# Kernel optimization log

Hardware: AMD Instinct MI355X
Metric: run time of the kernel (lower is better)

Reference implementation:

```python
import jax, jax.numpy as jnp
import numpy as np

NUM_Q = 4096     # num_of_questions
MAX_STEP = 256   # max_step
BATCH = 64       # students per batch


def setup_inputs() -> dict:
    key = jax.random.key(0)
    k1, k2, k3, k4, k5, k6 = jax.random.split(key, 6)
    # simulated interaction sequences with random leading padding (all-zero rows)
    q_ids = jax.random.randint(k1, (BATCH, MAX_STEP), 0, NUM_Q)
    correct = jax.random.bernoulli(k2, 0.6, (BATCH, MAX_STEP)).astype(jnp.float32)
    start = jax.random.randint(k3, (BATCH,), 0, 16)  # leading pad length per student
    valid = (jnp.arange(MAX_STEP)[None, :] >= start[:, None]).astype(jnp.float32)
    oh = jax.nn.one_hot(q_ids, NUM_Q, dtype=jnp.float32)  # [B,S,Q]
    # batch = [one-hot if answered correctly | one-hot if answered incorrectly]
    batch = jnp.concatenate(
        [oh * (correct * valid)[..., None], oh * ((1.0 - correct) * valid)[..., None]],
        axis=-1,
    )  # [B,S,2Q]
    pred = jax.random.uniform(k4, (BATCH, MAX_STEP, NUM_Q), minval=0.01, maxval=0.99)
    target_q = jax.random.uniform(k5, (BATCH, 1), minval=0.01, maxval=0.99)
    target_label = jax.random.bernoulli(k6, 0.5, (BATCH,)).astype(jnp.float32)
    return {"pred": pred, "target_q": target_q, "batch": batch, "target_label": target_label}


def _bce(p, a):
    # elementwise BCE matching torch.nn.BCELoss (log clamped at -100)
    logp = jnp.maximum(jnp.log(p), -100.0)
    log1mp = jnp.maximum(jnp.log1p(-p), -100.0)
    return -(a * logp + (1.0 - a) * log1mp)


def reference(pred, target_q, batch, target_label):
    Q, S = NUM_Q, MAX_STEP
    delta = batch[:, :, :Q] + batch[:, :, Q:]  # [B,S,Q] one-hot of asked question
    # temp.gather(0, arange) extracts the diagonal of pred[:S-1] @ delta[1:].T,
    # i.e. p[s,j] = pred[s,j] . delta[s,j+1]
    p = jnp.einsum('bsq,bsq->bs', pred[:, :S - 1], delta[:, 1:])  # [B,S-1]
    # correctness label: 1 if correct, 0 if incorrect or padded ('//' is non-diff)
    a = jax.lax.stop_gradient(
        jnp.floor(((batch[:, :, :Q] - batch[:, :, Q:]).sum(-1) + 1.0) / 2.0)
    )[:, 1:]  # [B,S-1]
    # the break loop trims everything before the first p[i] > 0;
    # if no p > 0, argmax returns 0 == no trim (matching torch, where break never fires)
    i = jnp.argmax(p > 0, axis=1)  # [B]
    mask = jnp.arange(S - 1)[None, :] >= i[:, None]
    seq_loss = jnp.sum(jnp.where(mask, _bce(p, a), 0.0), axis=1)  # [B]
    tail = _bce(target_q[:, 0], target_label)  # [B]
    # per-student mean over (trimmed length + 1 appended target)
    n = ((S - 1) - i + 1).astype(pred.dtype)
    return jnp.sum((seq_loss + tail) / n)
```

## Files before the change

### kernel.cpp

```cpp
#include <hip/hip_runtime.h>
#include <limits.h>

#define NUM_Q    4096
#define MAX_STEP 256
#define BATCH    64
#define TWOQ     8192

__global__ void __launch_bounds__(256) find_onehot_kernel(
        const float* __restrict__ batch, int* __restrict__ qa) {
    const int row = blockIdx.x;
    const float4* rp = (const float4*)(batch + (size_t)row * TWOQ);

    __shared__ int found;
    if (threadIdx.x == 0) found = -1;
    __syncthreads();

    #pragma unroll
    for (int it = 0; it < 8; ++it) {
        const int vi = it * 256 + threadIdx.x;
        const float4 v = rp[vi];
        if (v.x != 0.f || v.y != 0.f || v.z != 0.f || v.w != 0.f) {
            const int base = vi * 4;
            int idx = (v.x != 0.f) ? base
                    : (v.y != 0.f) ? base + 1
                    : (v.z != 0.f) ? base + 2
                                   : base + 3;
            found = idx;
        }
    }
    __syncthreads();
    if (threadIdx.x == 0) qa[row] = found;
}

__device__ __forceinline__ float bce(float p, float a) {
    float lp  = fmaxf(logf(p), -100.0f);
    float l1p = fmaxf(log1pf(-p), -100.0f);
    return -(a * lp + (1.0f - a) * l1p);
}

__global__ void __launch_bounds__(256) loss_kernel(
        const float* __restrict__ pred,
        const float* __restrict__ target_q,
        const float* __restrict__ target_label,
        const int* __restrict__ qa,
        float* __restrict__ out) {
    const int b = blockIdx.x;
    const int t = threadIdx.x;
    const int SM1 = MAX_STEP - 1;

    __shared__ int   smin[256];
    __shared__ float ssum[256];

    int   idx = -1;
    float p   = 0.0f;
    float a   = 0.0f;
    if (t < SM1) {
        idx = qa[b * MAX_STEP + t + 1];
        if (idx >= 0) {
            const int qid = idx & (NUM_Q - 1);
            p = pred[((size_t)b * MAX_STEP + t) * NUM_Q + qid];
            a = (idx < NUM_Q) ? 1.0f : 0.0f;
        }
    }

    smin[t] = (t < SM1 && idx >= 0 && p > 0.0f) ? t : INT_MAX;
    __syncthreads();
    #pragma unroll
    for (int off = 128; off > 0; off >>= 1) {
        if (t < off) smin[t] = min(smin[t], smin[t + off]);
        __syncthreads();
    }
    const int i0 = (smin[0] == INT_MAX) ? 0 : smin[0];

    float v = 0.0f;
    if (t < SM1 && t >= i0) v = bce(p, a);
    ssum[t] = v;
    __syncthreads();
    #pragma unroll
    for (int off = 128; off > 0; off >>= 1) {
        if (t < off) ssum[t] += ssum[t + off];
        __syncthreads();
    }

    if (t == 0) {
        const float tail = bce(target_q[b], target_label[b]);
        const float n = (float)(MAX_STEP - i0);
        atomicAdd(out, (ssum[0] + tail) / n);
    }
}

extern "C" void kernel_launch(void* const* d_in, const int* in_sizes, int n_in,
                              void* d_out, int out_size, void* d_ws, size_t ws_size,
                              hipStream_t stream) {
    const float* pred         = (const float*)d_in[0];
    const float* target_q     = (const float*)d_in[1];
    const float* batch        = (const float*)d_in[2];
    const float* target_label = (const float*)d_in[3];
    float* out = (float*)d_out;
    int*   qa  = (int*)d_ws;

    hipMemsetAsync(out, 0, (size_t)out_size * sizeof(float), stream);
    find_onehot_kernel<<<BATCH * MAX_STEP, 256, 0, stream>>>(batch, qa);
    loss_kernel<<<BATCH, 256, 0, stream>>>(pred, target_q, target_label, qa, out);
}
```

Before: 769.9 us.

## Scan one-hot rows per wavefront with ballot early-exit instead of full block scan

The one-hot search kernel now assigns one 64-lane wavefront per batch row instead of one 256-thread block. Lanes scan float4 chunks with a one-ahead prefetch and use a ballot to stop at the first nonzero chunk, broadcasting the index with a shuffle. This avoids reading the rest of each 32 KB row after the hit and removes shared memory and block barriers. Lane-serial iteration per row lowers parallelism per row, and padded rows still read the whole row. Detection uses the sum of the four values being positive, which relies on the one-hot entries being non-negative.

```diff
diff --git a/kernel.cpp b/kernel.cpp
--- a/kernel.cpp
+++ b/kernel.cpp
@@ -5,31 +5,42 @@
 #define MAX_STEP 256
 #define BATCH    64
 #define TWOQ     8192
+#define ROWS     (BATCH * MAX_STEP)
+#define VEC_PER_ROW (TWOQ / 4)
+#define ITERS    (VEC_PER_ROW / 64)
 
 __global__ void __launch_bounds__(256) find_onehot_kernel(
         const float* __restrict__ batch, int* __restrict__ qa) {
-    const int row = blockIdx.x;
+    const int gtid = blockIdx.x * blockDim.x + threadIdx.x;
+    const int row  = gtid >> 6;
+    const int lane = gtid & 63;
+    if (row >= ROWS) return;
+
     const float4* rp = (const float4*)(batch + (size_t)row * TWOQ);
 
-    __shared__ int found;
-    if (threadIdx.x == 0) found = -1;
-    __syncthreads();
-
-    #pragma unroll
-    for (int it = 0; it < 8; ++it) {
-        const int vi = it * 256 + threadIdx.x;
-        const float4 v = rp[vi];
-        if (v.x != 0.f || v.y != 0.f || v.z != 0.f || v.w != 0.f) {
-            const int base = vi * 4;
-            int idx = (v.x != 0.f) ? base
+    int found = -1;
+    float4 v = rp[lane];
+    for (int it = 0; it < ITERS; ++it) {
+        float4 nv;
+        if (it + 1 < ITERS) nv = rp[(it + 1) * 64 + lane];
+        const float s = v.x + v.y + v.z + v.w;
+        const unsigned long long m = __ballot(s > 0.0f);
+        if (m) {
+            const int src = __ffsll(m) - 1;
+            int idx = 0;
+            if (lane == src) {
+                const int base = (it * 64 + lane) * 4;
+                idx = (v.x != 0.f) ? base
                     : (v.y != 0.f) ? base + 1
                     : (v.z != 0.f) ? base + 2
                                    : base + 3;
-            found = idx;
+            }
+            found = __shfl(idx, src);
+            break;
         }
+        v = nv;
     }
-    __syncthreads();
-    if (threadIdx.x == 0) qa[row] = found;
+    if (lane == 0) qa[row] = found;
 }
 
 __device__ __forceinline__ float bce(float p, float a) {
@@ -100,6 +111,6 @@
     int*   qa  = (int*)d_ws;
 
     hipMemsetAsync(out, 0, (size_t)out_size * sizeof(float), stream);
-    find_onehot_kernel<<<BATCH * MAX_STEP, 256, 0, stream>>>(batch, qa);
+    find_onehot_kernel<<<(ROWS * 64) / 256, 256, 0, stream>>>(batch, qa);
     loss_kernel<<<BATCH, 256, 0, stream>>>(pred, target_q, target_label, qa, out);
 }
```

After: 733.4 us. 4.8% less time.
